# Kernel tuning notes

Hardware: AMD Instinct MI355X
Metric: run time of the kernel (lower is better)

## Reference

```python
import jax, jax.numpy as jnp
import numpy as np

EPS = 1e-5

def l2norm(x, axis=-1):
    # matches torch F.normalize(p=2): denom clamped at 1e-12
    n = jnp.linalg.norm(x, axis=axis, keepdims=True)
    return x / jnp.maximum(n, 1e-12)

def setup_inputs() -> dict:
    key = jax.random.key(0)
    ks = jax.random.split(key, 10)
    B, N, D, P = 8, 1024, 128, 16
    context = jax.random.normal(ks[0], (B, N, D), jnp.float32)
    acc_u = jax.random.normal(ks[1], (B, N, 1), jnp.float32)
    acc_v = jax.random.normal(ks[2], (B, N, 1), jnp.float32)
    uv_angle = jax.random.normal(ks[3], (B, N, 1), jnp.float32)
    uv_angleACC = jax.random.normal(ks[4], (B, N, 1), jnp.float32)
    speed = jax.random.normal(ks[5], (B, N, 1), jnp.float32)
    dist = jax.random.uniform(ks[6], (N, N), jnp.float32)
    angle = jax.random.normal(ks[7], (N, N), jnp.float32)
    # xavier_uniform for weight_tensor [P, D]: bound = sqrt(6/(P+D))
    bound = float(np.sqrt(6.0 / (P + D)))
    weight_tensor = jax.random.uniform(ks[8], (P, D), jnp.float32, -bound, bound)
    return {"context": context, "acc_u": acc_u, "acc_v": acc_v,
            "uv_angle": uv_angle, "uv_angleACC": uv_angleACC, "speed": speed,
            "isPhy": 1, "dist": dist, "angle": angle,
            "weight_tensor": weight_tensor}

def reference(context, acc_u, acc_v, uv_angle, uv_angleACC, speed, isPhy, dist, angle, weight_tensor):
    gamma, theta, sigma = 1.4, 0.5, 0.5
    P = weight_tensor.shape[0]
    N = context.shape[1]
    # --- weighted-cosine multi-perspective attention ---
    w = weight_tensor[:, None, None, :]                 # [P,1,1,D]
    context_fc = context[None] * w                      # [P,B,N,D]
    context_norm = l2norm(context_fc)                   # [P,B,N,D]
    # matmul over perspectives then mean over P
    attention = jnp.einsum('pbnd,pbmd->bnm', context_norm, context_norm) / P
    # --- epsilon neighbourhood (epsilon=0, markoff=0), mask detached ---
    mask = jax.lax.stop_gradient((attention > 0.0).astype(attention.dtype))
    attention = attention * mask
    # --- wind dynamics (pred_var 'u', isPhy True, dist given) ---
    Acc = acc_u * acc_u + acc_v * acc_v                 # [B,N,1]
    x1 = jnp.sqrt(Acc[:, :, 0] + EPS)                   # [B,N]
    x2 = jnp.abs(jnp.cos(uv_angleACC[:, :, 0] - uv_angle[:, :, 0]))
    temp_acc = x1 * x2                                  # [B,N]
    acc_part = temp_acc[:, :, None] * jnp.eye(N, dtype=attention.dtype)  # diag [B,N,N]
    spd = jax.lax.stop_gradient(speed)                  # speed.detach()
    ang = jax.lax.stop_gradient(angle)[None]            # torch.tensor() detaches
    d = jax.lax.stop_gradient(dist)[None] + EPS
    # uv_angle/speed broadcast [B,N,1] -> [B,N,N] (repeat along last dim)
    selfwind = jnp.abs(spd) * jnp.abs(jnp.cos(ang - uv_angle) + sigma * acc_part) / d
    selfwind = l2norm(selfwind)                         # [B,N,N]
    y = gamma * jnp.einsum('bnk,bmk->bnm', selfwind, selfwind) / 20.0 + EPS
    y = l2norm(y)
    u = l2norm(jnp.abs(theta * selfwind + jnp.sqrt(y)) + EPS)
    return attention * u
```

## Files before the change

kernel.cpp:

```cpp
#include <hip/hip_runtime.h>
#include <hip/hip_bf16.h>
#include <math.h>

#define EPSV 1e-5f
#define AS1 __attribute__((address_space(1)))
#define AS3 __attribute__((address_space(3)))

typedef __attribute__((ext_vector_type(4))) float f32x4;
typedef __attribute__((ext_vector_type(8))) short bf16x8;
typedef __attribute__((ext_vector_type(4))) unsigned short u16x4;

__device__ __forceinline__ unsigned short f2b(float x) {
  union { float f; unsigned int u; } v; v.f = x;
  unsigned int r = v.u + 0x7FFFu + ((v.u >> 16) & 1u);
  return (unsigned short)(r >> 16);
}
__device__ __forceinline__ float b2f(unsigned short h) {
  union { float f; unsigned int u; } v; v.u = ((unsigned int)h) << 16;
  return v.f;
}

__device__ __forceinline__ float block_reduce_sum(float v, float* sbuf) {
  #pragma unroll
  for (int off = 32; off; off >>= 1) v += __shfl_xor(v, off);
  __syncthreads();
  if ((threadIdx.x & 63) == 0) sbuf[threadIdx.x >> 6] = v;
  __syncthreads();
  return sbuf[0] + sbuf[1] + sbuf[2] + sbuf[3];
}

__global__ __launch_bounds__(256) void prep(const float* __restrict__ ctx,
                                            const float* __restrict__ wt,
                                            const float* __restrict__ speed,
                                            const float* __restrict__ uva,
                                            const float* __restrict__ accu,
                                            const float* __restrict__ accv,
                                            const float* __restrict__ uvaACC,
                                            const float* __restrict__ angle,
                                            const float* __restrict__ dist,
                                            unsigned short* __restrict__ V,
                                            unsigned short* __restrict__ SW,
                                            int BN, int N) {
  __shared__ float sbuf[4];
  const int blk = blockIdx.x;
  if (blk < BN) {
    const int bn = blk;
    const int w = threadIdx.x >> 6;
    const int lane = threadIdx.x & 63;
    const int p = w * 4 + (lane >> 4);
    const int dl = (lane & 15) * 8;
    const float* c = ctx + (size_t)bn * 128;
    const f32x4 ca = *(const f32x4*)(c + dl);
    const f32x4 cb = *(const f32x4*)(c + dl + 4);
    const f32x4 wa = *(const f32x4*)(wt + p * 128 + dl);
    const f32x4 wb = *(const f32x4*)(wt + p * 128 + dl + 4);
    float a[8];
    float ss = 0.0f;
    #pragma unroll
    for (int i = 0; i < 4; ++i) {
      a[i] = ca[i] * wa[i];
      a[4 + i] = cb[i] * wb[i];
      ss += a[i] * a[i] + a[4 + i] * a[4 + i];
    }
    ss += __shfl_xor(ss, 1);
    ss += __shfl_xor(ss, 2);
    ss += __shfl_xor(ss, 4);
    ss += __shfl_xor(ss, 8);
    const float inv = 1.0f / fmaxf(sqrtf(ss), 1e-12f);
    bf16x8 o;
    #pragma unroll
    for (int i = 0; i < 8; ++i) o[i] = (short)f2b(a[i] * inv);
    *(bf16x8*)(V + (size_t)bn * 2048 + p * 128 + dl) = o;
  } else {
    const int bn = blk - BN;
    const int n = bn & (N - 1);
    const int t = threadIdx.x;
    const float ua = uva[bn];
    const float sp = fabsf(speed[bn]);
    const float au = accu[bn], av = accv[bn];
    const float ta = sqrtf(au * au + av * av + EPSV) * fabsf(cosf(uvaACC[bn] - ua));
    const f32x4 an = *(const f32x4*)(angle + (size_t)n * N + 4 * t);
    const f32x4 dv = *(const f32x4*)(dist + (size_t)n * N + 4 * t);
    float v[4];
    float ss = 0.0f;
    #pragma unroll
    for (int i = 0; i < 4; ++i) {
      float cv = cosf(an[i] - ua);
      if (4 * t + i == n) cv += 0.5f * ta;
      v[i] = sp * fabsf(cv) / (dv[i] + EPSV);
      ss += v[i] * v[i];
    }
    ss = block_reduce_sum(ss, sbuf);
    const float inv = 1.0f / fmaxf(sqrtf(ss), 1e-12f);
    u16x4 o;
    #pragma unroll
    for (int i = 0; i < 4; ++i) o[i] = f2b(v[i] * inv);
    *(u16x4*)(SW + (size_t)bn * N + 4 * t) = o;
  }
}

#define FENCE asm volatile("" ::: "memory")
__device__ __forceinline__ void barx() { FENCE; __builtin_amdgcn_s_barrier(); FENCE; }

__global__ __launch_bounds__(512, 4) void gemm8(const unsigned short* __restrict__ V,
                                                const unsigned short* __restrict__ SW,
                                                float* __restrict__ OUT,
                                                unsigned short* __restrict__ Yb,
                                                int boff) {
  __shared__ __align__(16) unsigned short As[3][128 * 32];
  __shared__ __align__(16) unsigned short Bs[3][256 * 32];
  const int id = blockIdx.x + boff;
  const bool att = id < 256;
  const int r = att ? id : id - 256;
  const int b = r & 7;
  const int tile = r >> 3;
  const int m0 = (tile & 7) * 128;
  const int n0 = (tile >> 3) * 256;
  const int K = att ? 2048 : 1024;
  const int NN = 1024;
  const unsigned short* Ab = att ? (V + (size_t)b * NN * 2048) : (SW + (size_t)b * NN * NN);

  const int tid = threadIdx.x;
  const int lane = tid & 63;
  const int wid = tid >> 6;
  const int wm = (wid >> 2) * 64;
  const int wn = (wid & 3) * 64;
  const int fr = lane & 15;
  const int fc = lane >> 4;
  const int rsw = (fc ^ ((fr >> 1) & 3)) << 3;

  f32x4 acc[4][4] = {};
  bf16x8 af[4], bf[4];

  auto stage = [&](int sb, int kt) {
    const int k0 = kt << 5;
    {
      const int row = tid >> 2;
      const int c = (tid & 3) ^ ((row >> 1) & 3);
      __builtin_amdgcn_global_load_lds(
          (const AS1 unsigned int*)(Ab + (size_t)(m0 + row) * K + k0 + (c << 3)),
          (AS3 unsigned int*)(&As[sb][tid * 8]), 16, 0, 0);
    }
    #pragma unroll
    for (int e = 0; e < 2; ++e) {
      const int idx = e * 512 + tid;
      const int row = idx >> 2;
      const int c = (idx & 3) ^ ((row >> 1) & 3);
      __builtin_amdgcn_global_load_lds(
          (const AS1 unsigned int*)(Ab + (size_t)(n0 + row) * K + k0 + (c << 3)),
          (AS3 unsigned int*)(&Bs[sb][idx * 8]), 16, 0, 0);
    }
  };

  const int nk = K >> 5;

  stage(0, 0);
  stage(1, 1);
  asm volatile("s_waitcnt vmcnt(3)" ::: "memory");
  barx();

  int rd = 0;
  for (int t = 0; t < nk; ++t) {
    const unsigned short* Ar = As[rd];
    const unsigned short* Br = Bs[rd];
    #pragma unroll
    for (int i = 0; i < 4; ++i)
      af[i] = *(const bf16x8*)(Ar + (wm + i * 16 + fr) * 32 + rsw);
    #pragma unroll
    for (int j = 0; j < 4; ++j)
      bf[j] = *(const bf16x8*)(Br + (wn + j * 16 + fr) * 32 + rsw);

    if (t + 2 < nk) {
      int st = rd + 2; if (st >= 3) st -= 3;
      stage(st, t + 2);
    }
    barx();
    asm volatile("s_waitcnt lgkmcnt(0)" ::: "memory");
    __builtin_amdgcn_s_setprio(1);
    #pragma unroll
    for (int i = 0; i < 4; ++i)
      #pragma unroll
      for (int j = 0; j < 4; ++j)
        acc[i][j] = __builtin_amdgcn_mfma_f32_16x16x32_bf16(af[i], bf[j], acc[i][j], 0, 0, 0);
    __builtin_amdgcn_s_setprio(0);
    if (t + 2 < nk)      { asm volatile("s_waitcnt vmcnt(3)" ::: "memory"); }
    else if (t + 1 < nk) { asm volatile("s_waitcnt vmcnt(0)" ::: "memory"); }
    barx();
    rd = (rd + 1 == 3) ? 0 : rd + 1;
  }

  if (att) {
    float* Cb = OUT + (size_t)b * NN * NN;
    #pragma unroll
    for (int i = 0; i < 4; ++i)
      #pragma unroll
      for (int rr = 0; rr < 4; ++rr) {
        const int row = m0 + wm + i * 16 + fc * 4 + rr;
        #pragma unroll
        for (int j = 0; j < 4; ++j) {
          const int col = n0 + wn + j * 16 + fr;
          Cb[(size_t)row * NN + col] = fmaxf(acc[i][j][rr] * (1.0f / 16.0f), 0.0f);
        }
      }
  } else {
    unsigned short* Cb = Yb + (size_t)b * NN * NN;
    #pragma unroll
    for (int i = 0; i < 4; ++i)
      #pragma unroll
      for (int rr = 0; rr < 4; ++rr) {
        const int row = m0 + wm + i * 16 + fc * 4 + rr;
        #pragma unroll
        for (int j = 0; j < 4; ++j) {
          const int col = n0 + wn + j * 16 + fr;
          Cb[(size_t)row * NN + col] = f2b(acc[i][j][rr] * (1.4f / 20.0f) + EPSV);
        }
      }
  }
}

__global__ __launch_bounds__(256) void finkern(const unsigned short* __restrict__ Yb,
                                               const unsigned short* __restrict__ SW,
                                               float* __restrict__ OUT,
                                               int N) {
  __shared__ float sbuf[4];
  const int bn = blockIdx.x;
  const int t = threadIdx.x;
  const unsigned short* y = Yb + (size_t)bn * N;
  const unsigned short* sw = SW + (size_t)bn * N;
  float* o = OUT + (size_t)bn * N;

  const u16x4 yraw = *(const u16x4*)(y + 4 * t);
  float yv[4];
  float ss = 0.0f;
  #pragma unroll
  for (int i = 0; i < 4; ++i) {
    yv[i] = b2f(yraw[i]);
    ss += yv[i] * yv[i];
  }
  ss = block_reduce_sum(ss, sbuf);
  const float invy = 1.0f / fmaxf(sqrtf(ss), 1e-12f);

  const u16x4 swv = *(const u16x4*)(sw + 4 * t);
  float tv[4];
  float st = 0.0f;
  #pragma unroll
  for (int i = 0; i < 4; ++i) {
    tv[i] = fabsf(0.5f * b2f(swv[i]) + sqrtf(yv[i] * invy)) + EPSV;
    st += tv[i] * tv[i];
  }
  st = block_reduce_sum(st, sbuf);
  const float invt = 1.0f / fmaxf(sqrtf(st), 1e-12f);

  f32x4 ov = *(f32x4*)(o + 4 * t);
  #pragma unroll
  for (int i = 0; i < 4; ++i) ov[i] *= tv[i] * invt;
  *(f32x4*)(o + 4 * t) = ov;
}

extern "C" void kernel_launch(void* const* d_in, const int* in_sizes, int n_in,
                              void* d_out, int out_size, void* d_ws, size_t ws_size,
                              hipStream_t stream) {
  const float* ctx        = (const float*)d_in[0];
  const float* acc_u      = (const float*)d_in[1];
  const float* acc_v      = (const float*)d_in[2];
  const float* uv_angle   = (const float*)d_in[3];
  const float* uv_angleACC= (const float*)d_in[4];
  const float* speed      = (const float*)d_in[5];
  const float* dist       = (const float*)d_in[7];
  const float* angle      = (const float*)d_in[8];
  const float* wt         = (const float*)d_in[9];

  const int B = 8, N = 1024, P = 16;
  const int K1 = P * 128;
  const int BN = B * N;

  const size_t szV  = (size_t)BN * K1 * 2;
  const size_t szSW = (size_t)BN * N * 2;
  const size_t szYb = (size_t)BN * N * 2;

  unsigned short* V  = (unsigned short*)d_ws;
  unsigned short* SW = (unsigned short*)((char*)d_ws + szV);
  float* out = (float*)d_out;

  prep<<<dim3(2 * BN), dim3(256), 0, stream>>>(ctx, wt, speed, uv_angle, acc_u,
                                               acc_v, uv_angleACC, angle, dist,
                                               V, SW, BN, N);

  if (ws_size >= szV + szSW + szYb) {
    unsigned short* Yp = (unsigned short*)((char*)d_ws + szV + szSW);
    gemm8<<<dim3(512), dim3(512), 0, stream>>>(V, SW, out, Yp, 0);
    finkern<<<dim3(BN), dim3(256), 0, stream>>>(Yp, SW, out, N);
  } else {
    unsigned short* Yp = (unsigned short*)d_ws;
    gemm8<<<dim3(256), dim3(512), 0, stream>>>(V, SW, out, Yp, 0);
    gemm8<<<dim3(256), dim3(512), 0, stream>>>(V, SW, out, Yp, 256);
    finkern<<<dim3(BN), dim3(256), 0, stream>>>(Yp, SW, out, N);
  }
}
```

Before: 172.0 us.

## Restructure GEMM into 128x128 tiles computing both products per block; wave-per-row finalize

The GEMM kernel moves from 512-thread blocks with 128x256 tiles to 256-thread blocks with 128x128 tiles. Each block now runs the attention product and the selfwind Gram product in sequence, so there are 512 blocks that each do both segments instead of blocks split by role. The prefetch is reordered to issue before the LDS fragment reads, and the separate LDS wait is dropped. The finalize kernel assigns one wavefront per row and reduces with shuffles only, so no shared-memory block reduction is needed. This aims to balance load and cut sync overhead, at the cost of less reuse per tile and a longer serial run per block.

Result: slower. 184.1 us (+7.0%).

```diff
diff --git a/kernel.cpp b/kernel.cpp
--- a/kernel.cpp
+++ b/kernel.cpp
@@ -102,95 +102,89 @@
 #define FENCE asm volatile("" ::: "memory")
 __device__ __forceinline__ void barx() { FENCE; __builtin_amdgcn_s_barrier(); FENCE; }
 
-__global__ __launch_bounds__(512, 4) void gemm8(const unsigned short* __restrict__ V,
+__global__ __launch_bounds__(256, 2) void gemm2(const unsigned short* __restrict__ V,
                                                 const unsigned short* __restrict__ SW,
                                                 float* __restrict__ OUT,
                                                 unsigned short* __restrict__ Yb,
-                                                int boff) {
+                                                int mode) {
   __shared__ __align__(16) unsigned short As[3][128 * 32];
-  __shared__ __align__(16) unsigned short Bs[3][256 * 32];
-  const int id = blockIdx.x + boff;
-  const bool att = id < 256;
-  const int r = att ? id : id - 256;
-  const int b = r & 7;
-  const int tile = r >> 3;
+  __shared__ __align__(16) unsigned short Bs[3][128 * 32];
+  const int id = blockIdx.x;
+  const int b = id & 7;
+  const int tile = id >> 3;
   const int m0 = (tile & 7) * 128;
-  const int n0 = (tile >> 3) * 256;
-  const int K = att ? 2048 : 1024;
-  const int NN = 1024;
-  const unsigned short* Ab = att ? (V + (size_t)b * NN * 2048) : (SW + (size_t)b * NN * NN);
-
+  const int n0 = (tile >> 3) * 128;
   const int tid = threadIdx.x;
   const int lane = tid & 63;
   const int wid = tid >> 6;
-  const int wm = (wid >> 2) * 64;
-  const int wn = (wid & 3) * 64;
+  const int wm = (wid >> 1) * 64;
+  const int wn = (wid & 1) * 64;
   const int fr = lane & 15;
   const int fc = lane >> 4;
   const int rsw = (fc ^ ((fr >> 1) & 3)) << 3;
 
-  f32x4 acc[4][4] = {};
+  f32x4 acc[4][4];
   bf16x8 af[4], bf[4];
 
-  auto stage = [&](int sb, int kt) {
-    const int k0 = kt << 5;
-    {
-      const int row = tid >> 2;
-      const int c = (tid & 3) ^ ((row >> 1) & 3);
-      __builtin_amdgcn_global_load_lds(
-          (const AS1 unsigned int*)(Ab + (size_t)(m0 + row) * K + k0 + (c << 3)),
-          (AS3 unsigned int*)(&As[sb][tid * 8]), 16, 0, 0);
-    }
-    #pragma unroll
-    for (int e = 0; e < 2; ++e) {
-      const int idx = e * 512 + tid;
-      const int row = idx >> 2;
-      const int c = (idx & 3) ^ ((row >> 1) & 3);
-      __builtin_amdgcn_global_load_lds(
-          (const AS1 unsigned int*)(Ab + (size_t)(n0 + row) * K + k0 + (c << 3)),
-          (AS3 unsigned int*)(&Bs[sb][idx * 8]), 16, 0, 0);
+  auto runseg = [&](const unsigned short* Ab, int K) {
+    #pragma unroll
+    for (int i = 0; i < 4; ++i)
+      #pragma unroll
+      for (int j = 0; j < 4; ++j) acc[i][j] = f32x4{0.f, 0.f, 0.f, 0.f};
+
+    auto stage = [&](int sb, int kt) {
+      const int k0 = kt << 5;
+      #pragma unroll
+      for (int e = 0; e < 2; ++e) {
+        const int idx = e * 256 + tid;
+        const int row = idx >> 2;
+        const int c = (idx & 3) ^ ((row >> 1) & 3);
+        __builtin_amdgcn_global_load_lds(
+            (const AS1 unsigned int*)(Ab + (size_t)(m0 + row) * K + k0 + (c << 3)),
+            (AS3 unsigned int*)(&As[sb][idx * 8]), 16, 0, 0);
+        __builtin_amdgcn_global_load_lds(
+            (const AS1 unsigned int*)(Ab + (size_t)(n0 + row) * K + k0 + (c << 3)),
+            (AS3 unsigned int*)(&Bs[sb][idx * 8]), 16, 0, 0);
+      }
+    };
+
+    const int nk = K >> 5;
+    stage(0, 0);
+    stage(1, 1);
+    asm volatile("s_waitcnt vmcnt(4)" ::: "memory");
+    barx();
+
+    int rd = 0;
+    for (int t = 0; t < nk; ++t) {
+      if (t + 2 < nk) {
+        int st = rd + 2; if (st >= 3) st -= 3;
+        stage(st, t + 2);
+      }
+      const unsigned short* Ar = As[rd];
+      const unsigned short* Br = Bs[rd];
+      #pragma unroll
+      for (int i = 0; i < 4; ++i)
+        af[i] = *(const bf16x8*)(Ar + (wm + i * 16 + fr) * 32 + rsw);
+      #pragma unroll
+      for (int j = 0; j < 4; ++j)
+        bf[j] = *(const bf16x8*)(Br + (wn + j * 16 + fr) * 32 + rsw);
+      __builtin_amdgcn_s_setprio(1);
+      #pragma unroll
+      for (int i = 0; i < 4; ++i)
+        #pragma unroll
+        for (int j = 0; j < 4; ++j)
+          acc[i][j] = __builtin_amdgcn_mfma_f32_16x16x32_bf16(af[i], bf[j], acc[i][j], 0, 0, 0);
+      __builtin_amdgcn_s_setprio(0);
+      if (t + 2 < nk)      { asm volatile("s_waitcnt vmcnt(4)" ::: "memory"); }
+      else if (t + 1 < nk) { asm volatile("s_waitcnt vmcnt(0)" ::: "memory"); }
+      barx();
+      rd = (rd + 1 == 3) ? 0 : rd + 1;
     }
   };
 
-  const int nk = K >> 5;
-
-  stage(0, 0);
-  stage(1, 1);
-  asm volatile("s_waitcnt vmcnt(3)" ::: "memory");
-  barx();
-
-  int rd = 0;
-  for (int t = 0; t < nk; ++t) {
-    const unsigned short* Ar = As[rd];
-    const unsigned short* Br = Bs[rd];
-    #pragma unroll
-    for (int i = 0; i < 4; ++i)
-      af[i] = *(const bf16x8*)(Ar + (wm + i * 16 + fr) * 32 + rsw);
-    #pragma unroll
-    for (int j = 0; j < 4; ++j)
-      bf[j] = *(const bf16x8*)(Br + (wn + j * 16 + fr) * 32 + rsw);
-
-    if (t + 2 < nk) {
-      int st = rd + 2; if (st >= 3) st -= 3;
-      stage(st, t + 2);
-    }
-    barx();
-    asm volatile("s_waitcnt lgkmcnt(0)" ::: "memory");
-    __builtin_amdgcn_s_setprio(1);
-    #pragma unroll
-    for (int i = 0; i < 4; ++i)
-      #pragma unroll
-      for (int j = 0; j < 4; ++j)
-        acc[i][j] = __builtin_amdgcn_mfma_f32_16x16x32_bf16(af[i], bf[j], acc[i][j], 0, 0, 0);
-    __builtin_amdgcn_s_setprio(0);
-    if (t + 2 < nk)      { asm volatile("s_waitcnt vmcnt(3)" ::: "memory"); }
-    else if (t + 1 < nk) { asm volatile("s_waitcnt vmcnt(0)" ::: "memory"); }
-    barx();
-    rd = (rd + 1 == 3) ? 0 : rd + 1;
-  }
-
-  if (att) {
-    float* Cb = OUT + (size_t)b * NN * NN;
+  if (mode != 2) {
+    runseg(V + (size_t)b * 1024 * 2048, 2048);
+    float* Cb = OUT + (size_t)b * 1024 * 1024;
     #pragma unroll
     for (int i = 0; i < 4; ++i)
       #pragma unroll
@@ -199,11 +193,13 @@
         #pragma unroll
         for (int j = 0; j < 4; ++j) {
           const int col = n0 + wn + j * 16 + fr;
-          Cb[(size_t)row * NN + col] = fmaxf(acc[i][j][rr] * (1.0f / 16.0f), 0.0f);
+          Cb[(size_t)row * 1024 + col] = fmaxf(acc[i][j][rr] * (1.0f / 16.0f), 0.0f);
         }
       }
-  } else {
-    unsigned short* Cb = Yb + (size_t)b * NN * NN;
+  }
+  if (mode != 1) {
+    runseg(SW + (size_t)b * 1024 * 1024, 1024);
+    unsigned short* Cb = Yb + (size_t)b * 1024 * 1024;
     #pragma unroll
     for (int i = 0; i < 4; ++i)
       #pragma unroll
@@ -212,7 +208,7 @@
         #pragma unroll
         for (int j = 0; j < 4; ++j) {
           const int col = n0 + wn + j * 16 + fr;
-          Cb[(size_t)row * NN + col] = f2b(acc[i][j][rr] * (1.4f / 20.0f) + EPSV);
+          Cb[(size_t)row * 1024 + col] = f2b(acc[i][j][rr] * (1.4f / 20.0f) + EPSV);
         }
       }
   }
@@ -220,41 +216,51 @@
 
 __global__ __launch_bounds__(256) void finkern(const unsigned short* __restrict__ Yb,
                                                const unsigned short* __restrict__ SW,
-                                               float* __restrict__ OUT,
-                                               int N) {
-  __shared__ float sbuf[4];
-  const int bn = blockIdx.x;
-  const int t = threadIdx.x;
-  const unsigned short* y = Yb + (size_t)bn * N;
-  const unsigned short* sw = SW + (size_t)bn * N;
-  float* o = OUT + (size_t)bn * N;
-
-  const u16x4 yraw = *(const u16x4*)(y + 4 * t);
-  float yv[4];
+                                               float* __restrict__ OUT) {
+  const int row = blockIdx.x * 4 + (threadIdx.x >> 6);
+  const int lane = threadIdx.x & 63;
+  const unsigned short* y = Yb + (size_t)row * 1024;
+  const unsigned short* sw = SW + (size_t)row * 1024;
+  float* o = OUT + (size_t)row * 1024;
+
+  float yv[16];
   float ss = 0.0f;
   #pragma unroll
-  for (int i = 0; i < 4; ++i) {
-    yv[i] = b2f(yraw[i]);
-    ss += yv[i] * yv[i];
-  }
-  ss = block_reduce_sum(ss, sbuf);
+  for (int ch = 0; ch < 4; ++ch) {
+    const u16x4 yr = *(const u16x4*)(y + ch * 256 + lane * 4);
+    #pragma unroll
+    for (int i = 0; i < 4; ++i) {
+      yv[ch * 4 + i] = b2f(yr[i]);
+      ss += yv[ch * 4 + i] * yv[ch * 4 + i];
+    }
+  }
+  #pragma unroll
+  for (int off = 32; off; off >>= 1) ss += __shfl_xor(ss, off);
   const float invy = 1.0f / fmaxf(sqrtf(ss), 1e-12f);
 
-  const u16x4 swv = *(const u16x4*)(sw + 4 * t);
-  float tv[4];
+  float tv[16];
   float st = 0.0f;
   #pragma unroll
-  for (int i = 0; i < 4; ++i) {
-    tv[i] = fabsf(0.5f * b2f(swv[i]) + sqrtf(yv[i] * invy)) + EPSV;
-    st += tv[i] * tv[i];
-  }
-  st = block_reduce_sum(st, sbuf);
+  for (int ch = 0; ch < 4; ++ch) {
+    const u16x4 sr = *(const u16x4*)(sw + ch * 256 + lane * 4);
+    #pragma unroll
+    for (int i = 0; i < 4; ++i) {
+      const float x = fabsf(0.5f * b2f(sr[i]) + sqrtf(yv[ch * 4 + i] * invy)) + EPSV;
+      tv[ch * 4 + i] = x;
+      st += x * x;
+    }
+  }
+  #pragma unroll
+  for (int off = 32; off; off >>= 1) st += __shfl_xor(st, off);
   const float invt = 1.0f / fmaxf(sqrtf(st), 1e-12f);
 
-  f32x4 ov = *(f32x4*)(o + 4 * t);
-  #pragma unroll
-  for (int i = 0; i < 4; ++i) ov[i] *= tv[i] * invt;
-  *(f32x4*)(o + 4 * t) = ov;
+  #pragma unroll
+  for (int ch = 0; ch < 4; ++ch) {
+    f32x4 ov = *(f32x4*)(o + ch * 256 + lane * 4);
+    #pragma unroll
+    for (int i = 0; i < 4; ++i) ov[i] *= tv[ch * 4 + i] * invt;
+    *(f32x4*)(o + ch * 256 + lane * 4) = ov;
+  }
 }
 
 extern "C" void kernel_launch(void* const* d_in, const int* in_sizes, int n_in,
@@ -288,12 +294,12 @@
 
   if (ws_size >= szV + szSW + szYb) {
     unsigned short* Yp = (unsigned short*)((char*)d_ws + szV + szSW);
-    gemm8<<<dim3(512), dim3(512), 0, stream>>>(V, SW, out, Yp, 0);
-    finkern<<<dim3(BN), dim3(256), 0, stream>>>(Yp, SW, out, N);
+    gemm2<<<dim3(512), dim3(256), 0, stream>>>(V, SW, out, Yp, 0);
+    finkern<<<dim3(BN / 4), dim3(256), 0, stream>>>(Yp, SW, out);
   } else {
     unsigned short* Yp = (unsigned short*)d_ws;
-    gemm8<<<dim3(256), dim3(512), 0, stream>>>(V, SW, out, Yp, 0);
-    gemm8<<<dim3(256), dim3(512), 0, stream>>>(V, SW, out, Yp, 256);
-    finkern<<<dim3(BN), dim3(256), 0, stream>>>(Yp, SW, out, N);
-  }
-}
+    gemm2<<<dim3(512), dim3(256), 0, stream>>>(V, SW, out, Yp, 1);
+    gemm2<<<dim3(512), dim3(256), 0, stream>>>(V, SW, out, Yp, 2);
+    finkern<<<dim3(BN / 4), dim3(256), 0, stream>>>(Yp, SW, out);
+  }
+}
```

## Precompute cos/sin-over-dist tables and use wave-per-row final normalization

Applied to the files above, without the earlier changes.

A new kernel computes cos(angle)/dist and sin(angle)/dist once per N×N element with fast sincos. The selfwind prep then uses the angle-addition identity with a per-row sincos of uv_angle, replacing a full-precision cosf and a divide on every element of every batch. The final normalization kernel now gives each row to one 64-lane wave, reducing with shuffles only and no block barriers. The cost is an extra launch, 8 MB of table traffic, and lower accuracy from the fast sincos approximation. The fallback path also places the tables past the workspace regions, which may exceed a smaller workspace.

Measured after the change: 173.3 us. No clear change (+0.7%).

```diff
diff --git a/kernel.cpp b/kernel.cpp
--- a/kernel.cpp
+++ b/kernel.cpp
@@ -27,6 +27,26 @@
   if ((threadIdx.x & 63) == 0) sbuf[threadIdx.x >> 6] = v;
   __syncthreads();
   return sbuf[0] + sbuf[1] + sbuf[2] + sbuf[3];
+}
+
+__global__ __launch_bounds__(256) void tabkern(const float* __restrict__ angle,
+                                               const float* __restrict__ dist,
+                                               float* __restrict__ CT,
+                                               float* __restrict__ ST) {
+  const int i = (blockIdx.x * 256 + threadIdx.x) * 4;
+  const f32x4 a = *(const f32x4*)(angle + i);
+  const f32x4 d = *(const f32x4*)(dist + i);
+  f32x4 ct, st;
+  #pragma unroll
+  for (int j = 0; j < 4; ++j) {
+    const float inv = 1.0f / (d[j] + EPSV);
+    float s, c;
+    __sincosf(a[j], &s, &c);
+    ct[j] = c * inv;
+    st[j] = s * inv;
+  }
+  *(f32x4*)(CT + i) = ct;
+  *(f32x4*)(ST + i) = st;
 }
 
 __global__ __launch_bounds__(256) void prep(const float* __restrict__ ctx,
@@ -36,7 +56,8 @@
                                             const float* __restrict__ accu,
                                             const float* __restrict__ accv,
                                             const float* __restrict__ uvaACC,
-                                            const float* __restrict__ angle,
+                                            const float* __restrict__ CT,
+                                            const float* __restrict__ ST,
                                             const float* __restrict__ dist,
                                             unsigned short* __restrict__ V,
                                             unsigned short* __restrict__ SW,
@@ -76,18 +97,21 @@
     const int n = bn & (N - 1);
     const int t = threadIdx.x;
     const float ua = uva[bn];
+    float su, cu;
+    __sincosf(ua, &su, &cu);
     const float sp = fabsf(speed[bn]);
     const float au = accu[bn], av = accv[bn];
     const float ta = sqrtf(au * au + av * av + EPSV) * fabsf(cosf(uvaACC[bn] - ua));
-    const f32x4 an = *(const f32x4*)(angle + (size_t)n * N + 4 * t);
-    const f32x4 dv = *(const f32x4*)(dist + (size_t)n * N + 4 * t);
+    const float diag = 0.5f * ta / (dist[(size_t)n * N + n] + EPSV);
+    const f32x4 ct = *(const f32x4*)(CT + (size_t)n * N + 4 * t);
+    const f32x4 st = *(const f32x4*)(ST + (size_t)n * N + 4 * t);
     float v[4];
     float ss = 0.0f;
     #pragma unroll
     for (int i = 0; i < 4; ++i) {
-      float cv = cosf(an[i] - ua);
-      if (4 * t + i == n) cv += 0.5f * ta;
-      v[i] = sp * fabsf(cv) / (dv[i] + EPSV);
+      float x = cu * ct[i] + su * st[i];
+      if (4 * t + i == n) x += diag;
+      v[i] = sp * fabsf(x);
       ss += v[i] * v[i];
     }
     ss = block_reduce_sum(ss, sbuf);
@@ -220,41 +244,51 @@
 
 __global__ __launch_bounds__(256) void finkern(const unsigned short* __restrict__ Yb,
                                                const unsigned short* __restrict__ SW,
-                                               float* __restrict__ OUT,
-                                               int N) {
-  __shared__ float sbuf[4];
-  const int bn = blockIdx.x;
-  const int t = threadIdx.x;
-  const unsigned short* y = Yb + (size_t)bn * N;
-  const unsigned short* sw = SW + (size_t)bn * N;
-  float* o = OUT + (size_t)bn * N;
-
-  const u16x4 yraw = *(const u16x4*)(y + 4 * t);
-  float yv[4];
+                                               float* __restrict__ OUT) {
+  const int row = blockIdx.x * 4 + (threadIdx.x >> 6);
+  const int lane = threadIdx.x & 63;
+  const unsigned short* y = Yb + (size_t)row * 1024;
+  const unsigned short* sw = SW + (size_t)row * 1024;
+  float* o = OUT + (size_t)row * 1024;
+
+  float yv[16];
   float ss = 0.0f;
   #pragma unroll
-  for (int i = 0; i < 4; ++i) {
-    yv[i] = b2f(yraw[i]);
-    ss += yv[i] * yv[i];
-  }
-  ss = block_reduce_sum(ss, sbuf);
+  for (int ch = 0; ch < 4; ++ch) {
+    const u16x4 yr = *(const u16x4*)(y + ch * 256 + lane * 4);
+    #pragma unroll
+    for (int i = 0; i < 4; ++i) {
+      yv[ch * 4 + i] = b2f(yr[i]);
+      ss += yv[ch * 4 + i] * yv[ch * 4 + i];
+    }
+  }
+  #pragma unroll
+  for (int off = 32; off; off >>= 1) ss += __shfl_xor(ss, off);
   const float invy = 1.0f / fmaxf(sqrtf(ss), 1e-12f);
 
-  const u16x4 swv = *(const u16x4*)(sw + 4 * t);
-  float tv[4];
+  float tv[16];
   float st = 0.0f;
   #pragma unroll
-  for (int i = 0; i < 4; ++i) {
-    tv[i] = fabsf(0.5f * b2f(swv[i]) + sqrtf(yv[i] * invy)) + EPSV;
-    st += tv[i] * tv[i];
-  }
-  st = block_reduce_sum(st, sbuf);
+  for (int ch = 0; ch < 4; ++ch) {
+    const u16x4 sr = *(const u16x4*)(sw + ch * 256 + lane * 4);
+    #pragma unroll
+    for (int i = 0; i < 4; ++i) {
+      const float x = fabsf(0.5f * b2f(sr[i]) + sqrtf(yv[ch * 4 + i] * invy)) + EPSV;
+      tv[ch * 4 + i] = x;
+      st += x * x;
+    }
+  }
+  #pragma unroll
+  for (int off = 32; off; off >>= 1) st += __shfl_xor(st, off);
   const float invt = 1.0f / fmaxf(sqrtf(st), 1e-12f);
 
-  f32x4 ov = *(f32x4*)(o + 4 * t);
-  #pragma unroll
-  for (int i = 0; i < 4; ++i) ov[i] *= tv[i] * invt;
-  *(f32x4*)(o + 4 * t) = ov;
+  #pragma unroll
+  for (int ch = 0; ch < 4; ++ch) {
+    f32x4 ov = *(f32x4*)(o + ch * 256 + lane * 4);
+    #pragma unroll
+    for (int i = 0; i < 4; ++i) ov[i] *= tv[ch * 4 + i] * invt;
+    *(f32x4*)(o + ch * 256 + lane * 4) = ov;
+  }
 }
 
 extern "C" void kernel_launch(void* const* d_in, const int* in_sizes, int n_in,
@@ -277,23 +311,36 @@
   const size_t szV  = (size_t)BN * K1 * 2;
   const size_t szSW = (size_t)BN * N * 2;
   const size_t szYb = (size_t)BN * N * 2;
+  const size_t szT  = (size_t)N * N * 4;
 
   unsigned short* V  = (unsigned short*)d_ws;
   unsigned short* SW = (unsigned short*)((char*)d_ws + szV);
   float* out = (float*)d_out;
 
-  prep<<<dim3(2 * BN), dim3(256), 0, stream>>>(ctx, wt, speed, uv_angle, acc_u,
-                                               acc_v, uv_angleACC, angle, dist,
-                                               V, SW, BN, N);
-
   if (ws_size >= szV + szSW + szYb) {
-    unsigned short* Yp = (unsigned short*)((char*)d_ws + szV + szSW);
+    char* region3 = (char*)d_ws + szV + szSW;
+    float* CT = (float*)region3;
+    float* ST = (float*)(region3 + szT);
+    unsigned short* Yp = (unsigned short*)region3;
+
+    tabkern<<<dim3(N * N / 1024), dim3(256), 0, stream>>>(angle, dist, CT, ST);
+    prep<<<dim3(2 * BN), dim3(256), 0, stream>>>(ctx, wt, speed, uv_angle, acc_u,
+                                                 acc_v, uv_angleACC, CT, ST, dist,
+                                                 V, SW, BN, N);
     gemm8<<<dim3(512), dim3(512), 0, stream>>>(V, SW, out, Yp, 0);
-    finkern<<<dim3(BN), dim3(256), 0, stream>>>(Yp, SW, out, N);
+    finkern<<<dim3(BN / 4), dim3(256), 0, stream>>>(Yp, SW, out);
   } else {
+    char* tabs = (char*)d_ws + szV + szSW;
+    float* CT = (float*)tabs;
+    float* ST = (float*)(tabs + szT);
     unsigned short* Yp = (unsigned short*)d_ws;
+
+    tabkern<<<dim3(N * N / 1024), dim3(256), 0, stream>>>(angle, dist, CT, ST);
+    prep<<<dim3(2 * BN), dim3(256), 0, stream>>>(ctx, wt, speed, uv_angle, acc_u,
+                                                 acc_v, uv_angleACC, CT, ST, dist,
+                                                 V, SW, BN, N);
     gemm8<<<dim3(256), dim3(512), 0, stream>>>(V, SW, out, Yp, 0);
     gemm8<<<dim3(256), dim3(512), 0, stream>>>(V, SW, out, Yp, 256);
-    finkern<<<dim3(BN), dim3(256), 0, stream>>>(Yp, SW, out, N);
-  }
-}
+    finkern<<<dim3(BN / 4), dim3(256), 0, stream>>>(Yp, SW, out);
+  }
+}
```
